# Optimization experiments

Measured on AMD Instinct MI355X. Metric: run time of the kernel, lower is better.

The kernel has to match this reference:

```python
import jax, jax.numpy as jnp
import numpy as np

N, E, CIN, H, HEADS, B = 50000, 800000, 16, 64, 3, 64
D0 = HEADS * H            # conv1 out (heads concatenated) = 192
D1 = D0 + CIN             # x1 dim = 208
D2 = 2 * D1               # x2 dim = 416
MLP_IN = 3 * D2           # 1248
MLP_HID = MLP_IN // 2     # 624
EPS = 1e-5


def setup_inputs() -> dict:
    key = jax.random.key(0)
    ks = jax.random.split(key, 24)
    r = lambda k, s, sc=0.05: (jax.random.normal(k, s, dtype=jnp.float32) * sc)
    inp = {
        'x': jax.random.normal(ks[0], (N, CIN), dtype=jnp.float32),
        'edge_index': jax.random.randint(ks[1], (2, E), 0, N, dtype=jnp.int32),
        'edge_attr': jax.random.normal(ks[2], (E, 4), dtype=jnp.float32),
        'batch': jnp.sort(jax.random.randint(ks[3], (N,), 0, B, dtype=jnp.int32)),
        # conv1 (GeneralConv, heads=3, concat): msg/edge/self linears -> D0
        'W_msg1': r(ks[4], (CIN, D0)), 'b_msg1': jnp.zeros((D0,), jnp.float32),
        'W_edge1': r(ks[5], (4, D0)), 'b_edge1': jnp.zeros((D0,), jnp.float32),
        'W_self1': r(ks[6], (CIN, D0)), 'b_self1': jnp.zeros((D0,), jnp.float32),
        'g1': jnp.ones((D0,), jnp.float32), 'be1': jnp.zeros((D0,), jnp.float32),
        # conv2 (GeneralConv, heads=1, in==out -> identity self)
        'W_msg2': r(ks[7], (D1, D1)), 'b_msg2': jnp.zeros((D1,), jnp.float32),
        'W_edge2': r(ks[8], (4, D1)), 'b_edge2': jnp.zeros((D1,), jnp.float32),
        'g2': jnp.ones((D1,), jnp.float32), 'be2': jnp.zeros((D1,), jnp.float32),
        # MLP head
        'W_l1': r(ks[9], (MLP_IN, MLP_HID)), 'b_l1': jnp.zeros((MLP_HID,), jnp.float32),
        'alpha': jnp.asarray(0.25, jnp.float32),  # PReLU default
        'W_l2': r(ks[10], (MLP_HID, 2)), 'b_l2': jnp.zeros((2,), jnp.float32),
    }
    return inp


def _bn(h, g, b):
    m = h.mean(axis=0)
    v = h.var(axis=0)  # biased, like torch BatchNorm training mode
    return (h - m) * jax.lax.rsqrt(v + EPS) * g + b


def reference(x, edge_index, edge_attr, batch,
              W_msg1, b_msg1, W_edge1, b_edge1, W_self1, b_self1, g1, be1,
              W_msg2, b_msg2, W_edge2, b_edge2, g2, be2,
              W_l1, b_l1, alpha, W_l2, b_l2):
    src, dst = edge_index[0], edge_index[1]
    # conv1: gather -> linear msg + edge feature -> scatter-add -> + self linear
    m1 = x[src] @ W_msg1 + b_msg1 + edge_attr @ W_edge1 + b_edge1   # [E, D0]
    h1 = jax.ops.segment_sum(m1, dst, num_segments=N) + (x @ W_self1 + b_self1)
    h1 = _bn(h1, g1, be1)
    x1 = jnp.concatenate([h1, x], axis=1)                           # [N, D1]
    # conv2 (identity self-connection since in==out)
    m2 = x1[src] @ W_msg2 + b_msg2 + edge_attr @ W_edge2 + b_edge2  # [E, D1]
    h2 = jax.ops.segment_sum(m2, dst, num_segments=N) + x1
    h2 = _bn(h2, g2, be2)
    x2 = jnp.concatenate([h2, x1], axis=1)                          # [N, D2]
    # global add / mean / max pooling by graph id
    s = jax.ops.segment_sum(x2, batch, num_segments=B)
    cnt = jax.ops.segment_sum(jnp.ones((x2.shape[0], 1), x2.dtype), batch, num_segments=B)
    mean = s / jnp.maximum(cnt, 1.0)
    mx = jax.ops.segment_max(x2, batch, num_segments=B)
    pooled = jnp.concatenate([s, mx, mean], axis=1)                 # [B, 3*D2]
    # MLP head: Linear -> Dropout(0) -> PReLU -> Linear -> log_softmax
    h = pooled @ W_l1 + b_l1
    h = jnp.where(h >= 0, h, alpha * h)
    logits = h @ W_l2 + b_l2
    return jax.nn.log_softmax(logits, axis=-1)
```

## Files before the change

### kernel.cpp

```cpp
#include <hip/hip_runtime.h>

typedef __attribute__((ext_vector_type(8))) short short8;
typedef __attribute__((ext_vector_type(4))) float f32x4;
typedef unsigned short u16;
typedef unsigned int u32;

__device__ __forceinline__ u16 f2bf(float f) {
  u32 u = __float_as_uint(f);
  u = (u + 0x7fffu + ((u >> 16) & 1u)) >> 16;
  return (u16)u;
}
__device__ __forceinline__ float bf2f(u16 v) { return __uint_as_float((u32)v << 16); }
__device__ __forceinline__ void atomAddF(float* p, float v) { unsafeAtomicAdd(p, v); }
__device__ __forceinline__ void addp(float* v, u32 p) {
  v[0] += bf2f((u16)p);
  v[1] += bf2f((u16)(p >> 16));
}
__device__ __forceinline__ u32 encf(float f) {
  u32 u = __float_as_uint(f);
  return (u & 0x80000000u) ? ~u : (u | 0x80000000u);
}
__device__ __forceinline__ float decf(u32 u) {
  return (u & 0x80000000u) ? __uint_as_float(u ^ 0x80000000u) : __uint_as_float(~u);
}

__global__ void prep_k(const float* __restrict__ Wm1, const float* __restrict__ We1,
                       const float* __restrict__ Ws1, const float* __restrict__ Wm2,
                       const float* __restrict__ Wl1, const float* __restrict__ x,
                       const int* __restrict__ batch, u16* __restrict__ Wp1,
                       u16* __restrict__ Wp2, u16* __restrict__ Wp3,
                       u16* __restrict__ xbf, int* __restrict__ gstart,
                       int* __restrict__ gend, int* __restrict__ deg,
                       float* __restrict__ bns1p, float* __restrict__ bns2p,
                       float* __restrict__ psumg, u32* __restrict__ pmaxg,
                       u32* __restrict__ pming, int N, int E) {
  int tid = blockIdx.x * 256 + threadIdx.x;
  if (tid < 64 * 192) {
    int k = tid / 192, n = tid % 192;
    float v = 0.f;
    if (k < 16) v = Wm1[k * 192 + n];
    else if (k < 20) v = We1[(k - 16) * 192 + n];
    else if (k < 36) v = Ws1[(k - 20) * 192 + n];
    Wp1[((k >> 3) * 192 + n) * 8 + (k & 7)] = f2bf(v);
  }
  if (tid < 224 * 208) {
    int k = tid / 208, n = tid % 208;
    float v = (k < 208) ? Wm2[k * 208 + n] : 0.f;
    Wp2[((k >> 3) * 208 + n) * 8 + (k & 7)] = f2bf(v);
  }
  if (tid < N * 8) {
    float2 p = *(const float2*)(x + (size_t)tid * 2);
    *(u32*)(xbf + (size_t)tid * 2) = (u32)f2bf(p.x) | ((u32)f2bf(p.y) << 16);
  }
  if (tid < N) {
    int b = batch[tid];
    if (tid == 0 || batch[tid - 1] != b) gstart[b] = tid;
    if (tid == N - 1 || batch[tid + 1] != b) gend[b] = tid;
    deg[tid] = 0;
  }
  if (tid < 64 * 384) bns1p[tid] = 0.f;
  if (tid < 64 * 832) bns2p[tid] = 0.f;
  if (tid < 64 * 416) {
    psumg[tid] = 0.f;
    pmaxg[tid] = 0x007FFFFFu;
    pming[tid] = 0xFF800000u;
  }
  if (tid < 1248 * 624) {
    int k = tid / 624, n = tid % 624;
    Wp3[((size_t)(k >> 3) * 624 + n) * 8 + (k & 7)] = f2bf(Wl1[(size_t)k * 624 + n]);
  }
}

__global__ void count_k(const int* __restrict__ ei, int* __restrict__ deg,
                        int* __restrict__ ord, int E) {
  int e = blockIdx.x * 256 + threadIdx.x;
  if (e >= E) return;
  ord[e] = atomicAdd(&deg[ei[E + e]], 1);
}

__global__ void scanA_k(const int* __restrict__ deg, int* __restrict__ bsum, int N) {
  __shared__ int sh[256];
  int t = threadIdx.x;
  int i = blockIdx.x * 256 + t;
  sh[t] = (i < N) ? deg[i] : 0;
  __syncthreads();
  for (int off = 128; off > 0; off >>= 1) {
    if (t < off) sh[t] += sh[t + off];
    __syncthreads();
  }
  if (t == 0) bsum[blockIdx.x] = sh[0];
}

__global__ void scanC_k(const int* __restrict__ deg, const int* __restrict__ bsum,
                        int* __restrict__ rowptr, int N, int nb) {
  __shared__ int sb2[256];
  __shared__ int sh[256];
  int t = threadIdx.x;
  int bv = (t < nb) ? bsum[t] : 0;
  sb2[t] = bv;
  __syncthreads();
  for (int off = 1; off < 256; off <<= 1) {
    int u = (t >= off) ? sb2[t - off] : 0;
    __syncthreads();
    sb2[t] += u;
    __syncthreads();
  }
  int bpref = (blockIdx.x == 0) ? 0 : sb2[blockIdx.x - 1];
  int i = blockIdx.x * 256 + t;
  int d = (i < N) ? deg[i] : 0;
  sh[t] = d;
  __syncthreads();
  for (int off = 1; off < 256; off <<= 1) {
    int u = (t >= off) ? sh[t - off] : 0;
    __syncthreads();
    sh[t] += u;
    __syncthreads();
  }
  int excl = sh[t] - d + bpref;
  if (i < N) {
    rowptr[i] = excl;
    if (i == N - 1) rowptr[N] = excl + d;
  }
}

__global__ void scatter_k(const int* __restrict__ ei, const float* __restrict__ ea,
                          const int* __restrict__ ord, const int* __restrict__ rowptr,
                          int4* __restrict__ se16, int E) {
  int e = blockIdx.x * 256 + threadIdx.x;
  if (e >= E) return;
  int s = ei[e], d = ei[E + e];
  float4 w = *(const float4*)(ea + (size_t)e * 4);
  int slot = rowptr[d] + ord[e];
  int4 ent;
  ent.x = s;
  ent.y = (int)((u32)f2bf(w.x) | ((u32)f2bf(w.y) << 16));
  ent.z = (int)((u32)f2bf(w.z) | ((u32)f2bf(w.w) << 16));
  ent.w = 0;
  se16[slot] = ent;
}

__global__ void __launch_bounds__(256) conv1_k(
    const int4* __restrict__ se16, const int* __restrict__ rowptr,
    const u16* __restrict__ xbf, const u16* __restrict__ Bp,
    const float* __restrict__ bm1, const float* __restrict__ be1,
    const float* __restrict__ bs1, u16* __restrict__ acc1c, u16* __restrict__ h1bf,
    float* __restrict__ bns1p, const int* __restrict__ batch,
    float* __restrict__ psumg, u32* __restrict__ pmaxg, u32* __restrict__ pming, int N) {
  __shared__ __align__(16) u16 Uls[16][72];
  __shared__ float degls[16];
  int tid = threadIdx.x;
  int nl = tid >> 4, q = tid & 15;
  int n = blockIdx.x * 16 + nl;
  bool nval = n < N;
  int j0 = nval ? rowptr[n] : 0;
  int j1 = nval ? rowptr[n + 1] : 0;
  int base = blockIdx.x * 16;
  int gid_lo = batch[base];
  int gid_hi = batch[min(base + 15, N - 1)];
  bool uni = (gid_lo == gid_hi);
  float v[20];
#pragma unroll
  for (int i = 0; i < 20; ++i) v[i] = 0.f;
  {
    int j = j0 + q;
    bool a0 = j < j1, a1 = (j + 16) < j1;
    int jj0 = a0 ? j : 0;
    int jj1 = a1 ? (j + 16) : 0;
    int4 p0 = se16[jj0];
    int4 p1 = se16[jj1];
    const uint4* xs0 = (const uint4*)(xbf + (size_t)(a0 ? p0.x : 0) * 16);
    uint4 x00 = xs0[0], x01 = xs0[1];
    const uint4* xs1 = (const uint4*)(xbf + (size_t)(a1 ? p1.x : 0) * 16);
    uint4 x10 = xs1[0], x11 = xs1[1];
    if (a0) {
      addp(v + 0, x00.x); addp(v + 2, x00.y); addp(v + 4, x00.z); addp(v + 6, x00.w);
      addp(v + 8, x01.x); addp(v + 10, x01.y); addp(v + 12, x01.z); addp(v + 14, x01.w);
      addp(v + 16, (u32)p0.y); addp(v + 18, (u32)p0.z);
    }
    if (a1) {
      addp(v + 0, x10.x); addp(v + 2, x10.y); addp(v + 4, x10.z); addp(v + 6, x10.w);
      addp(v + 8, x11.x); addp(v + 10, x11.y); addp(v + 12, x11.z); addp(v + 14, x11.w);
      addp(v + 16, (u32)p1.y); addp(v + 18, (u32)p1.z);
    }
    for (j += 32; j < j1; j += 16) {
      int4 p = se16[j];
      const uint4* xs = (const uint4*)(xbf + (size_t)p.x * 16);
      uint4 x0 = xs[0], x1 = xs[1];
      addp(v + 0, x0.x); addp(v + 2, x0.y); addp(v + 4, x0.z); addp(v + 6, x0.w);
      addp(v + 8, x1.x); addp(v + 10, x1.y); addp(v + 12, x1.z); addp(v + 14, x1.w);
      addp(v + 16, (u32)p.y); addp(v + 18, (u32)p.z);
    }
  }
#pragma unroll
  for (int i = 0; i < 20; ++i) {
    v[i] += __shfl_xor(v[i], 1);
    v[i] += __shfl_xor(v[i], 2);
    v[i] += __shfl_xor(v[i], 4);
    v[i] += __shfl_xor(v[i], 8);
  }
  float degf = (float)(j1 - j0);
  const u16* xr = xbf + (size_t)n * 16;
  {
    u32 w2[2];
#pragma unroll
    for (int jj = 0; jj < 2; ++jj) {
      int t0 = q * 4 + 2 * jj, t1 = t0 + 1;
      u16 b0 = (t0 < 20) ? f2bf(v[t0]) : ((t0 < 36 && nval) ? xr[t0 - 20] : (u16)0);
      u16 b1 = (t1 < 20) ? f2bf(v[t1]) : ((t1 < 36 && nval) ? xr[t1 - 20] : (u16)0);
      w2[jj] = (u32)b0 | ((u32)b1 << 16);
    }
    *(uint2*)&Uls[nl][q * 4] = make_uint2(w2[0], w2[1]);
  }
  if (nval) {
    int t0 = q * 2, t1 = t0 + 1;
    float f0 = (t0 < 20) ? v[t0] : ((t0 == 20) ? degf : 0.f);
    float f1 = (t1 < 20) ? v[t1] : ((t1 == 20) ? degf : 0.f);
    *(u32*)(acc1c + (size_t)n * 32 + q * 2) = (u32)f2bf(f0) | ((u32)f2bf(f1) << 16);
  }
  if (q == 0) degls[nl] = degf;
  __syncthreads();
  int w = tid >> 6, lane = tid & 63, rc = lane & 15, qd = lane >> 4;
  int slice = (blockIdx.x & 63) * 384;
  for (int nt = w; nt < 12; nt += 4) {
    f32x4 acc = {0.f, 0.f, 0.f, 0.f};
#pragma unroll
    for (int kb = 0; kb < 2; ++kb) {
      short8 av = *(const short8*)&Uls[rc][kb * 32 + qd * 8];
      short8 bv = *(const short8*)(Bp + (size_t)((kb * 4 + qd) * 192 + nt * 16 + rc) * 8);
      acc = __builtin_amdgcn_mfma_f32_16x16x32_bf16(av, bv, acc, 0, 0, 0);
    }
    int col = nt * 16 + rc;
    float bb = bm1[col] + be1[col], bsv = bs1[col];
    float ps = 0.f, pq = 0.f;
    float sl = 0.f, mxl = -3.4e38f, mnl = 3.4e38f;
    float vv[4];
#pragma unroll
    for (int r = 0; r < 4; ++r) {
      int ml = qd * 4 + r;
      int m = blockIdx.x * 16 + ml;
      float val = acc[r] + degls[ml] * bb + bsv;
      u16 vb = f2bf(val);
      float vr = bf2f(vb);
      vv[r] = vr;
      if (m < N) {
        h1bf[(size_t)m * 192 + col] = vb;
        ps += val;
        pq += val * val;
        sl += vr;
        mxl = fmaxf(mxl, vr);
        mnl = fminf(mnl, vr);
      }
    }
    ps += __shfl_xor(ps, 16); ps += __shfl_xor(ps, 32);
    pq += __shfl_xor(pq, 16); pq += __shfl_xor(pq, 32);
    if (uni) {
      sl += __shfl_xor(sl, 16); sl += __shfl_xor(sl, 32);
      mxl = fmaxf(mxl, __shfl_xor(mxl, 16)); mxl = fmaxf(mxl, __shfl_xor(mxl, 32));
      mnl = fminf(mnl, __shfl_xor(mnl, 16)); mnl = fminf(mnl, __shfl_xor(mnl, 32));
    }
    if (qd == 0) {
      atomAddF(&bns1p[slice + col], ps);
      atomAddF(&bns1p[slice + 192 + col], pq);
      if (uni) {
        int pidx = gid_lo * 416 + 208 + col;
        atomAddF(&psumg[pidx], sl);
        atomicMax(&pmaxg[pidx], encf(mxl));
        atomicMin(&pming[pidx], encf(mnl));
      }
    }
    if (!uni) {
      int cg = -1;
      float rs = 0.f, rmx = -3.4e38f, rmn = 3.4e38f;
#pragma unroll
      for (int r = 0; r < 4; ++r) {
        int m = blockIdx.x * 16 + qd * 4 + r;
        if (m >= N) continue;
        int g = batch[m];
        if (g != cg) {
          if (cg >= 0) {
            int pidx = cg * 416 + 208 + col;
            atomAddF(&psumg[pidx], rs);
            atomicMax(&pmaxg[pidx], encf(rmx));
            atomicMin(&pming[pidx], encf(rmn));
          }
          cg = g; rs = 0.f; rmx = -3.4e38f; rmn = 3.4e38f;
        }
        rs += vv[r];
        rmx = fmaxf(rmx, vv[r]);
        rmn = fminf(rmn, vv[r]);
      }
      if (cg >= 0) {
        int pidx = cg * 416 + 208 + col;
        atomAddF(&psumg[pidx], rs);
        atomicMax(&pmaxg[pidx], encf(rmx));
        atomicMin(&pming[pidx], encf(rmn));
      }
    }
  }
  if (tid < 16) {
    int c = tid;
    int rows = min(16, N - base);
    if (uni) {
      float s = 0.f, mx = -3.4e38f, mn = 3.4e38f;
      for (int ml = 0; ml < rows; ++ml) {
        float vx = bf2f(Uls[ml][20 + c]);
        s += vx;
        mx = fmaxf(mx, vx);
        mn = fminf(mn, vx);
      }
      int pidx = gid_lo * 416 + 400 + c;
      atomAddF(&psumg[pidx], s);
      atomicMax(&pmaxg[pidx], encf(mx));
      atomicMin(&pming[pidx], encf(mn));
    } else {
      int cg = -1;
      float rs = 0.f, rmx = -3.4e38f, rmn = 3.4e38f;
      for (int ml = 0; ml < rows; ++ml) {
        int g = batch[base + ml];
        if (g != cg) {
          if (cg >= 0) {
            int pidx = cg * 416 + 400 + c;
            atomAddF(&psumg[pidx], rs);
            atomicMax(&pmaxg[pidx], encf(rmx));
            atomicMin(&pming[pidx], encf(rmn));
          }
          cg = g; rs = 0.f; rmx = -3.4e38f; rmn = 3.4e38f;
        }
        float vx = bf2f(Uls[ml][20 + c]);
        rs += vx;
        rmx = fmaxf(rmx, vx);
        rmn = fminf(rmn, vx);
      }
      if (cg >= 0) {
        int pidx = cg * 416 + 400 + c;
        atomAddF(&psumg[pidx], rs);
        atomicMax(&pmaxg[pidx], encf(rmx));
        atomicMin(&pming[pidx], encf(rmn));
      }
    }
  }
}

__global__ void bnfin1_k(const float* __restrict__ bns1p, const float* __restrict__ g1,
                         const float* __restrict__ bta1, float Ninv,
                         float* __restrict__ aff1) {
  int c = threadIdx.x;
  if (c >= 192) return;
  float sm = 0.f, sq = 0.f;
  for (int k = 0; k < 64; ++k) {
    sm += bns1p[k * 384 + c];
    sq += bns1p[k * 384 + 192 + c];
  }
  float m1 = sm * Ninv;
  float var = sq * Ninv - m1 * m1;
  float s1 = g1[c] * rsqrtf(var + 1e-5f);
  aff1[c] = s1;
  aff1[192 + c] = bta1[c] - m1 * s1;
}

__global__ void __launch_bounds__(256) conv2_k(
    const int4* __restrict__ se16, const int* __restrict__ rowptr,
    const u16* __restrict__ acc1c, const u16* __restrict__ h1bf,
    const u16* __restrict__ xbf, const u16* __restrict__ Bp1, const u16* __restrict__ Bp2,
    const float* __restrict__ bm1, const float* __restrict__ be1,
    const float* __restrict__ bs1, const float* __restrict__ aff1,
    const float* __restrict__ We2, const float* __restrict__ bm2,
    const float* __restrict__ be2, float* __restrict__ bns2p,
    const int* __restrict__ batch, float* __restrict__ psumg,
    u32* __restrict__ pmaxg, u32* __restrict__ pming, int N) {
  __shared__ __align__(16) u16 Uls[16][72];
  __shared__ __align__(16) u16 Vls[16][232];
  __shared__ __align__(16) u16 X1ls[16][208];
  __shared__ float degls[16], sdegls[16], eals[16][4];
  int tid = threadIdx.x;
  int nl = tid >> 4, q = tid & 15;
  int n = blockIdx.x * 16 + nl;
  bool nval = n < N;
  int j0 = nval ? rowptr[n] : 0;
  int j1 = nval ? rowptr[n + 1] : 0;
  int base = blockIdx.x * 16;
  int gid_lo = batch[base];
  int gid_hi = batch[min(base + 15, N - 1)];
  bool uni = (gid_lo == gid_hi);

  uint4 sg0, sg1, sgx;
  int r0 = tid / 24, c0 = tid % 24;
  int r1 = (tid + 256) / 24, c1 = (tid + 256) % 24;
  {
    int gr = base + r0;
    sg0 = (gr < N) ? *(const uint4*)(h1bf + (size_t)gr * 192 + c0 * 8)
                   : make_uint4(0, 0, 0, 0);
  }
  if (tid < 128) {
    int gr = base + r1;
    sg1 = (gr < N) ? *(const uint4*)(h1bf + (size_t)gr * 192 + c1 * 8)
                   : make_uint4(0, 0, 0, 0);
  }
  if (tid < 32) {
    int gr = base + (tid >> 1);
    sgx = (gr < N) ? *(const uint4*)(xbf + (size_t)gr * 16 + (tid & 1) * 8)
                   : make_uint4(0, 0, 0, 0);
  }

  float v[21];
#pragma unroll
  for (int i = 0; i < 21; ++i) v[i] = 0.f;
  {
    int j = j0 + q;
    bool a0 = j < j1, a1 = (j + 16) < j1;
    int jj0 = a0 ? j : 0;
    int jj1 = a1 ? (j + 16) : 0;
    int4 p0 = se16[jj0];
    int4 p1 = se16[jj1];
    const uint4* cr0 = (const uint4*)(acc1c + (size_t)(a0 ? p0.x : 0) * 32);
    uint4 c00 = cr0[0], c01 = cr0[1], c02 = cr0[2];
    const uint4* cr1 = (const uint4*)(acc1c + (size_t)(a1 ? p1.x : 0) * 32);
    uint4 c10 = cr1[0], c11 = cr1[1], c12 = cr1[2];
    if (a0) {
      addp(v + 0, c00.x); addp(v + 2, c00.y); addp(v + 4, c00.z); addp(v + 6, c00.w);
      addp(v + 8, c01.x); addp(v + 10, c01.y); addp(v + 12, c01.z); addp(v + 14, c01.w);
      addp(v + 16, c02.x); addp(v + 18, c02.y);
      v[20] += bf2f((u16)c02.z);
    }
    if (a1) {
      addp(v + 0, c10.x); addp(v + 2, c10.y); addp(v + 4, c10.z); addp(v + 6, c10.w);
      addp(v + 8, c11.x); addp(v + 10, c11.y); addp(v + 12, c11.z); addp(v + 14, c11.w);
      addp(v + 16, c12.x); addp(v + 18, c12.y);
      v[20] += bf2f((u16)c12.z);
    }
    for (j += 32; j < j1; j += 16) {
      int s = se16[j].x;
      const uint4* cr = (const uint4*)(acc1c + (size_t)s * 32);
      uint4 c0 = cr[0], c1 = cr[1], c2 = cr[2];
      addp(v + 0, c0.x); addp(v + 2, c0.y); addp(v + 4, c0.z); addp(v + 6, c0.w);
      addp(v + 8, c1.x); addp(v + 10, c1.y); addp(v + 12, c1.z); addp(v + 14, c1.w);
      addp(v + 16, c2.x); addp(v + 18, c2.y);
      v[20] += bf2f((u16)c2.z);
    }
  }

  *(uint4*)&X1ls[r0][c0 * 8] = sg0;
  if (tid < 128) *(uint4*)&X1ls[r1][c1 * 8] = sg1;
  if (tid < 32) *(uint4*)&X1ls[tid >> 1][192 + (tid & 1) * 8] = sgx;

#pragma unroll
  for (int i = 0; i < 21; ++i) {
    v[i] += __shfl_xor(v[i], 1);
    v[i] += __shfl_xor(v[i], 2);
    v[i] += __shfl_xor(v[i], 4);
    v[i] += __shfl_xor(v[i], 8);
  }
  const u16* selfr = acc1c + (size_t)n * 32;
  {
    u32 w2[2];
#pragma unroll
    for (int jj = 0; jj < 2; ++jj) {
      int t0 = q * 4 + 2 * jj, t1 = t0 + 1;
      u16 b0 = (t0 < 20) ? f2bf(v[t0]) : ((t0 < 36 && nval) ? selfr[t0 - 20] : (u16)0);
      u16 b1 = (t1 < 20) ? f2bf(v[t1]) : ((t1 < 36 && nval) ? selfr[t1 - 20] : (u16)0);
      w2[jj] = (u32)b0 | ((u32)b1 << 16);
    }
    *(uint2*)&Uls[nl][q * 4] = make_uint2(w2[0], w2[1]);
  }
  {
    int t0 = q * 2, t1 = t0 + 1;
    u16 b0 = (t0 < 16 && nval) ? selfr[t0] : (u16)0;
    u16 b1 = (t1 < 16 && nval) ? selfr[t1] : (u16)0;
    *(u32*)&Vls[nl][192 + q * 2] = (u32)b0 | ((u32)b1 << 16);
  }
  if (q == 0) sdegls[nl] = v[20];
  if (q == 1) degls[nl] = nval ? bf2f(selfr[20]) : 0.f;
  if (q == 2) {
#pragma unroll
    for (int k = 0; k < 4; ++k) eals[nl][k] = nval ? bf2f(selfr[16 + k]) : 0.f;
  }
  __syncthreads();
  int w = tid >> 6, lane = tid & 63, rc = lane & 15, qd = lane >> 4;
  for (int nt = w; nt < 12; nt += 4) {
    f32x4 acc = {0.f, 0.f, 0.f, 0.f};
#pragma unroll
    for (int kb = 0; kb < 2; ++kb) {
      short8 av = *(const short8*)&Uls[rc][kb * 32 + qd * 8];
      short8 bv = *(const short8*)(Bp1 + (size_t)((kb * 4 + qd) * 192 + nt * 16 + rc) * 8);
      acc = __builtin_amdgcn_mfma_f32_16x16x32_bf16(av, bv, acc, 0, 0, 0);
    }
    int col = nt * 16 + rc;
    float s1 = aff1[col], t1 = aff1[192 + col];
    float bb = bm1[col] + be1[col], bsv = bs1[col];
#pragma unroll
    for (int r = 0; r < 4; ++r) {
      int ml = qd * 4 + r;
      float qv = acc[r] + sdegls[ml] * bb + degls[ml] * bsv;
      Vls[ml][col] = f2bf(qv * s1 + degls[ml] * t1);
    }
  }
  __syncthreads();
  int slice = (blockIdx.x & 63) * 832;
  for (int nt = w; nt < 13; nt += 4) {
    f32x4 acc = {0.f, 0.f, 0.f, 0.f};
#pragma unroll
    for (int kb = 0; kb < 7; ++kb) {
      short8 av = *(const short8*)&Vls[rc][kb * 32 + qd * 8];
      short8 bv = *(const short8*)(Bp2 + (size_t)((kb * 4 + qd) * 208 + nt * 16 + rc) * 8);
      acc = __builtin_amdgcn_mfma_f32_16x16x32_bf16(av, bv, acc, 0, 0, 0);
    }
    int col = nt * 16 + rc;
    float w0 = We2[col], w1 = We2[208 + col], w2 = We2[416 + col], w3 = We2[624 + col];
    float bb2 = bm2[col] + be2[col];
    bool c192 = col < 192;
    float s1 = c192 ? aff1[col] : 0.f;
    float t1 = c192 ? aff1[192 + col] : 0.f;
    float ps = 0.f, pq = 0.f;
    float sl = 0.f, mxl = -3.4e38f, mnl = 3.4e38f;
    float vv[4];
#pragma unroll
    for (int r = 0; r < 4; ++r) {
      int ml = qd * 4 + r;
      int m = blockIdx.x * 16 + ml;
      bool mv = m < N;
      float x1 = bf2f(X1ls[ml][col]);
      if (c192) x1 = x1 * s1 + t1;
      float val = acc[r] + eals[ml][0] * w0 + eals[ml][1] * w1 + eals[ml][2] * w2 +
                  eals[ml][3] * w3 + degls[ml] * bb2 + x1;
      vv[r] = val;
      if (mv) {
        ps += val;
        pq += val * val;
        sl += val;
        mxl = fmaxf(mxl, val);
        mnl = fminf(mnl, val);
      }
    }
    ps += __shfl_xor(ps, 16); ps += __shfl_xor(ps, 32);
    pq += __shfl_xor(pq, 16); pq += __shfl_xor(pq, 32);
    if (uni) {
      sl += __shfl_xor(sl, 16); sl += __shfl_xor(sl, 32);
      mxl = fmaxf(mxl, __shfl_xor(mxl, 16)); mxl = fmaxf(mxl, __shfl_xor(mxl, 32));
      mnl = fminf(mnl, __shfl_xor(mnl, 16)); mnl = fminf(mnl, __shfl_xor(mnl, 32));
    }
    if (qd == 0) {
      atomAddF(&bns2p[slice + col], ps);
      atomAddF(&bns2p[slice + 416 + col], pq);
      if (uni) {
        int pidx = gid_lo * 416 + col;
        atomAddF(&psumg[pidx], sl);
        atomicMax(&pmaxg[pidx], encf(mxl));
        atomicMin(&pming[pidx], encf(mnl));
      }
    }
    if (!uni) {
      int cg = -1;
      float rs = 0.f, rmx = -3.4e38f, rmn = 3.4e38f;
#pragma unroll
      for (int r = 0; r < 4; ++r) {
        int m = blockIdx.x * 16 + qd * 4 + r;
        if (m >= N) continue;
        int g = batch[m];
        if (g != cg) {
          if (cg >= 0) {
            int pidx = cg * 416 + col;
            atomAddF(&psumg[pidx], rs);
            atomicMax(&pmaxg[pidx], encf(rmx));
            atomicMin(&pming[pidx], encf(rmn));
          }
          cg = g; rs = 0.f; rmx = -3.4e38f; rmn = 3.4e38f;
        }
        rs += vv[r];
        rmx = fmaxf(rmx, vv[r]);
        rmn = fminf(rmn, vv[r]);
      }
      if (cg >= 0) {
        int pidx = cg * 416 + col;
        atomAddF(&psumg[pidx], rs);
        atomicMax(&pmaxg[pidx], encf(rmx));
        atomicMin(&pming[pidx], encf(rmn));
      }
    }
  }
}

__global__ void pooledprep_k(const float* __restrict__ psumg, const u32* __restrict__ pmaxg,
                             const u32* __restrict__ pming,
                             const int* __restrict__ gstart, const int* __restrict__ gend,
                             const float* __restrict__ bns2p, const float* __restrict__ aff1,
                             const float* __restrict__ g2, const float* __restrict__ bta2,
                             float Ninv, u16* __restrict__ Apool) {
  __shared__ float scs[416], shs[416];
  int b = blockIdx.x, t = threadIdx.x;
  for (int f = t; f < 416; f += 256) {
    float sc, sh;
    if (f < 208) {
      float sm = 0.f, sq = 0.f;
      for (int k = 0; k < 64; ++k) {
        sm += bns2p[k * 832 + f];
        sq += bns2p[k * 832 + 416 + f];
      }
      float m2 = sm * Ninv;
      float var = sq * Ninv - m2 * m2;
      sc = g2[f] * rsqrtf(var + 1e-5f);
      sh = bta2[f] - m2 * sc;
    } else if (f < 400) {
      sc = aff1[f - 208];
      sh = aff1[192 + (f - 208)];
    } else {
      sc = 1.f;
      sh = 0.f;
    }
    scs[f] = sc;
    shs[f] = sh;
  }
  __syncthreads();
  int cnt = gend[b] - gstart[b] + 1;
  float inv = 1.f / (float)max(cnt, 1);
  for (int f = t; f < 416; f += 256) {
    float s = psumg[b * 416 + f];
    float mx = decf(pmaxg[b * 416 + f]);
    float mn = decf(pming[b * 416 + f]);
    float sc = scs[f], sh = shs[f];
    float sumf = sc * s + (float)cnt * sh;
    float mxf = (sc >= 0.f) ? sc * mx + sh : sc * mn + sh;
    u16* row = Apool + (size_t)b * 1248;
    row[f] = f2bf(sumf);
    row[416 + f] = f2bf((cnt > 0) ? mxf : 0.f);
    row[832 + f] = f2bf(sumf * inv);
  }
}

__global__ void __launch_bounds__(256) mlpgemm_k(const u16* __restrict__ A,
                                                 const u16* __restrict__ Bp,
                                                 const float* __restrict__ b1,
                                                 const float* __restrict__ al,
                                                 float* __restrict__ hid) {
  __shared__ __align__(16) float part[3][64][4];
  int tid = threadIdx.x;
  int w = tid >> 6, lane = tid & 63;
  int mt = blockIdx.x, nt = blockIdx.y;
  int rc = lane & 15, qd = lane >> 4;
  f32x4 acc = {0.f, 0.f, 0.f, 0.f};
  const u16* Ap = A + (size_t)(mt * 16 + rc) * 1248 + qd * 8;
  const u16* Bq = Bp + (size_t)(qd * 624 + nt * 16 + rc) * 8;
  for (int kb = w; kb < 39; kb += 4) {
    short8 av = *(const short8*)(Ap + kb * 32);
    short8 bv = *(const short8*)(Bq + (size_t)kb * 4 * 624 * 8);
    acc = __builtin_amdgcn_mfma_f32_16x16x32_bf16(av, bv, acc, 0, 0, 0);
  }
  if (w > 0) *(f32x4*)&part[w - 1][lane][0] = acc;
  __syncthreads();
  if (w == 0) {
#pragma unroll
    for (int j = 0; j < 3; ++j) {
      f32x4 p = *(const f32x4*)&part[j][lane][0];
      acc[0] += p[0]; acc[1] += p[1]; acc[2] += p[2]; acc[3] += p[3];
    }
    int col = nt * 16 + rc;
    float bb = b1[col], alpha = al[0];
    int m0 = mt * 16 + qd * 4;
#pragma unroll
    for (int r = 0; r < 4; ++r) {
      float v = acc[r] + bb;
      hid[(size_t)(m0 + r) * 624 + col] = (v >= 0.f) ? v : alpha * v;
    }
  }
}

__global__ void head_k(const float* __restrict__ hid, const float* __restrict__ W2,
                       const float* __restrict__ b2, float* __restrict__ out) {
  int b = blockIdx.x, t = threadIdx.x;
  float p0 = 0.f, p1 = 0.f;
  for (int k = t; k < 624; k += 64) {
    float h = hid[(size_t)b * 624 + k];
    p0 += h * W2[k * 2];
    p1 += h * W2[k * 2 + 1];
  }
#pragma unroll
  for (int off = 32; off > 0; off >>= 1) {
    p0 += __shfl_down(p0, off);
    p1 += __shfl_down(p1, off);
  }
  if (t == 0) {
    float l0 = p0 + b2[0], l1 = p1 + b2[1];
    float m = fmaxf(l0, l1);
    float lse = m + logf(expf(l0 - m) + expf(l1 - m));
    out[b * 2] = l0 - lse;
    out[b * 2 + 1] = l1 - lse;
  }
}

extern "C" void kernel_launch(void* const* d_in, const int* in_sizes, int n_in,
                              void* d_out, int out_size, void* d_ws, size_t ws_size,
                              hipStream_t stream) {
  const float* x = (const float*)d_in[0];
  const int* ei = (const int*)d_in[1];
  const float* ea = (const float*)d_in[2];
  const int* batch = (const int*)d_in[3];
  const float* Wm1 = (const float*)d_in[4];
  const float* bm1 = (const float*)d_in[5];
  const float* We1 = (const float*)d_in[6];
  const float* be1 = (const float*)d_in[7];
  const float* Ws1 = (const float*)d_in[8];
  const float* bs1 = (const float*)d_in[9];
  const float* g1 = (const float*)d_in[10];
  const float* bta1 = (const float*)d_in[11];
  const float* Wm2 = (const float*)d_in[12];
  const float* bm2 = (const float*)d_in[13];
  const float* We2 = (const float*)d_in[14];
  const float* be2 = (const float*)d_in[15];
  const float* g2 = (const float*)d_in[16];
  const float* bta2 = (const float*)d_in[17];
  const float* Wl1 = (const float*)d_in[18];
  const float* bl1 = (const float*)d_in[19];
  const float* alpha = (const float*)d_in[20];
  const float* Wl2 = (const float*)d_in[21];
  const float* bl2 = (const float*)d_in[22];
  float* out = (float*)d_out;

  const int N = in_sizes[3];
  const int E = in_sizes[2] / 4;
  const int nb = (N + 255) / 256;
  const float Ninv = 1.f / (float)N;

  float* ws = (float*)d_ws;
  size_t o = 0;
  u16* acc1c = (u16*)(ws + o); o += (size_t)N * 16;
  u16* h1bf = (u16*)(ws + o);  o += (size_t)N * 96;
  u16* xbf = (u16*)(ws + o);   o += (size_t)N * 8;
  u16* Wp1 = (u16*)(ws + o);   o += 6144;
  u16* Wp2 = (u16*)(ws + o);   o += 23296;
  u16* Wp3 = (u16*)(ws + o);   o += 389376;
  u16* Apool = (u16*)(ws + o); o += 39936;
  float* hid = ws + o;    o += 64 * 624;
  float* bns1p = ws + o;  o += 64 * 384;
  float* bns2p = ws + o;  o += 64 * 832;
  float* aff1 = ws + o;   o += 384;
  float* psumg = ws + o;  o += 64 * 416;
  u32* pmaxg = (u32*)(ws + o); o += 64 * 416;
  u32* pming = (u32*)(ws + o); o += 64 * 416;
  int* gstart = (int*)(ws + o); o += 64;
  int* gend = (int*)(ws + o);   o += 64;
  int* deg = (int*)(ws + o);    o += N;
  int* rowptr = (int*)(ws + o); o += N + 1;
  int* ord = (int*)(ws + o);    o += E;
  int* bsum = (int*)(ws + o);   o += 256;
  o = (o + 3) & ~(size_t)3;
  int4* se16 = (int4*)(ws + o); o += (size_t)4 * E;

  const int gconv = (N + 15) / 16;
  prep_k<<<(E + 255) / 256, 256, 0, stream>>>(Wm1, We1, Ws1, Wm2, Wl1, x, batch, Wp1, Wp2,
                                              Wp3, xbf, gstart, gend, deg, bns1p, bns2p,
                                              psumg, pmaxg, pming, N, E);
  count_k<<<(E + 255) / 256, 256, 0, stream>>>(ei, deg, ord, E);
  scanA_k<<<nb, 256, 0, stream>>>(deg, bsum, N);
  scanC_k<<<nb, 256, 0, stream>>>(deg, bsum, rowptr, N, nb);
  scatter_k<<<(E + 255) / 256, 256, 0, stream>>>(ei, ea, ord, rowptr, se16, E);
  conv1_k<<<gconv, 256, 0, stream>>>(se16, rowptr, xbf, Wp1, bm1, be1, bs1, acc1c, h1bf,
                                     bns1p, batch, psumg, pmaxg, pming, N);
  bnfin1_k<<<1, 256, 0, stream>>>(bns1p, g1, bta1, Ninv, aff1);
  conv2_k<<<gconv, 256, 0, stream>>>(se16, rowptr, acc1c, h1bf, xbf, Wp1, Wp2, bm1, be1,
                                     bs1, aff1, We2, bm2, be2, bns2p, batch, psumg,
                                     pmaxg, pming, N);
  pooledprep_k<<<64, 256, 0, stream>>>(psumg, pmaxg, pming, gstart, gend, bns2p, aff1,
                                       g2, bta2, Ninv, Apool);
  mlpgemm_k<<<dim3(4, 39), 256, 0, stream>>>(Apool, Wp3, bl1, alpha, hid);
  head_k<<<64, 64, 0, stream>>>(hid, Wl2, bl2, out);
}
```

Baseline: 279.5 us.

## Fuse degree count into prep, single-pass scan, and pooled prep into MLP GEMM

Folds the edge degree counting into the prep kernel, with deg zeroed by a memset, and replaces the two-kernel block scan with one kernel in which each block recomputes its prefix by summing all earlier degrees. It also fuses the pooled-feature preparation into the MLP GEMM, building the bf16 A tile in shared memory per block. The aim is to cut kernel launches and the Apool global round trip. In exchange, each block in the scan and GEMM does redundant work (the prefix sum over earlier degrees, and the BN2 statistic reduction repeated in all 156 GEMM blocks).

```diff
diff --git a/kernel.cpp b/kernel.cpp
--- a/kernel.cpp
+++ b/kernel.cpp
@@ -27,10 +27,11 @@
 __global__ void prep_k(const float* __restrict__ Wm1, const float* __restrict__ We1,
                        const float* __restrict__ Ws1, const float* __restrict__ Wm2,
                        const float* __restrict__ Wl1, const float* __restrict__ x,
-                       const int* __restrict__ batch, u16* __restrict__ Wp1,
-                       u16* __restrict__ Wp2, u16* __restrict__ Wp3,
-                       u16* __restrict__ xbf, int* __restrict__ gstart,
-                       int* __restrict__ gend, int* __restrict__ deg,
+                       const int* __restrict__ batch, const int* __restrict__ ei,
+                       u16* __restrict__ Wp1, u16* __restrict__ Wp2,
+                       u16* __restrict__ Wp3, u16* __restrict__ xbf,
+                       int* __restrict__ gstart, int* __restrict__ gend,
+                       int* __restrict__ deg, int* __restrict__ ord,
                        float* __restrict__ bns1p, float* __restrict__ bns2p,
                        float* __restrict__ psumg, u32* __restrict__ pmaxg,
                        u32* __restrict__ pming, int N, int E) {
@@ -56,7 +57,6 @@
     int b = batch[tid];
     if (tid == 0 || batch[tid - 1] != b) gstart[b] = tid;
     if (tid == N - 1 || batch[tid + 1] != b) gend[b] = tid;
-    deg[tid] = 0;
   }
   if (tid < 64 * 384) bns1p[tid] = 0.f;
   if (tid < 64 * 832) bns2p[tid] = 0.f;
@@ -69,44 +69,26 @@
     int k = tid / 624, n = tid % 624;
     Wp3[((size_t)(k >> 3) * 624 + n) * 8 + (k & 7)] = f2bf(Wl1[(size_t)k * 624 + n]);
   }
-}
-
-__global__ void count_k(const int* __restrict__ ei, int* __restrict__ deg,
-                        int* __restrict__ ord, int E) {
-  int e = blockIdx.x * 256 + threadIdx.x;
-  if (e >= E) return;
-  ord[e] = atomicAdd(&deg[ei[E + e]], 1);
-}
-
-__global__ void scanA_k(const int* __restrict__ deg, int* __restrict__ bsum, int N) {
+  if (tid < E) {
+    ord[tid] = atomicAdd(&deg[ei[E + tid]], 1);
+  }
+}
+
+__global__ void scan_k(const int* __restrict__ deg, int* __restrict__ rowptr, int N) {
+  __shared__ int red[256];
   __shared__ int sh[256];
   int t = threadIdx.x;
-  int i = blockIdx.x * 256 + t;
-  sh[t] = (i < N) ? deg[i] : 0;
+  int start = blockIdx.x * 256;
+  int acc = 0;
+  for (int idx = t; idx < start; idx += 256) acc += deg[idx];
+  red[t] = acc;
   __syncthreads();
   for (int off = 128; off > 0; off >>= 1) {
-    if (t < off) sh[t] += sh[t + off];
+    if (t < off) red[t] += red[t + off];
     __syncthreads();
   }
-  if (t == 0) bsum[blockIdx.x] = sh[0];
-}
-
-__global__ void scanC_k(const int* __restrict__ deg, const int* __restrict__ bsum,
-                        int* __restrict__ rowptr, int N, int nb) {
-  __shared__ int sb2[256];
-  __shared__ int sh[256];
-  int t = threadIdx.x;
-  int bv = (t < nb) ? bsum[t] : 0;
-  sb2[t] = bv;
-  __syncthreads();
-  for (int off = 1; off < 256; off <<= 1) {
-    int u = (t >= off) ? sb2[t - off] : 0;
-    __syncthreads();
-    sb2[t] += u;
-    __syncthreads();
-  }
-  int bpref = (blockIdx.x == 0) ? 0 : sb2[blockIdx.x - 1];
-  int i = blockIdx.x * 256 + t;
+  int bpref = red[0];
+  int i = start + t;
   int d = (i < N) ? deg[i] : 0;
   sh[t] = d;
   __syncthreads();
@@ -579,15 +561,20 @@
   }
 }
 
-__global__ void pooledprep_k(const float* __restrict__ psumg, const u32* __restrict__ pmaxg,
-                             const u32* __restrict__ pming,
-                             const int* __restrict__ gstart, const int* __restrict__ gend,
-                             const float* __restrict__ bns2p, const float* __restrict__ aff1,
-                             const float* __restrict__ g2, const float* __restrict__ bta2,
-                             float Ninv, u16* __restrict__ Apool) {
+__global__ void __launch_bounds__(256) mlpgemm_k(
+    const float* __restrict__ psumg, const u32* __restrict__ pmaxg,
+    const u32* __restrict__ pming, const int* __restrict__ gstart,
+    const int* __restrict__ gend, const float* __restrict__ bns2p,
+    const float* __restrict__ aff1, const float* __restrict__ g2,
+    const float* __restrict__ bta2, float Ninv, const u16* __restrict__ Bp,
+    const float* __restrict__ b1, const float* __restrict__ al,
+    float* __restrict__ hid) {
   __shared__ float scs[416], shs[416];
-  int b = blockIdx.x, t = threadIdx.x;
-  for (int f = t; f < 416; f += 256) {
+  __shared__ __align__(16) u16 Als[16][1256];
+  __shared__ __align__(16) float part[3][64][4];
+  int tid = threadIdx.x;
+  int mt = blockIdx.x, nt = blockIdx.y;
+  for (int f = tid; f < 416; f += 256) {
     float sc, sh;
     if (f < 208) {
       float sm = 0.f, sq = 0.f;
@@ -610,37 +597,28 @@
     shs[f] = sh;
   }
   __syncthreads();
-  int cnt = gend[b] - gstart[b] + 1;
-  float inv = 1.f / (float)max(cnt, 1);
-  for (int f = t; f < 416; f += 256) {
+  for (int e = tid; e < 16 * 416; e += 256) {
+    int g = e / 416, f = e % 416;
+    int b = mt * 16 + g;
+    int cnt = gend[b] - gstart[b] + 1;
+    float inv = 1.f / (float)max(cnt, 1);
     float s = psumg[b * 416 + f];
     float mx = decf(pmaxg[b * 416 + f]);
     float mn = decf(pming[b * 416 + f]);
     float sc = scs[f], sh = shs[f];
     float sumf = sc * s + (float)cnt * sh;
     float mxf = (sc >= 0.f) ? sc * mx + sh : sc * mn + sh;
-    u16* row = Apool + (size_t)b * 1248;
-    row[f] = f2bf(sumf);
-    row[416 + f] = f2bf((cnt > 0) ? mxf : 0.f);
-    row[832 + f] = f2bf(sumf * inv);
-  }
-}
-
-__global__ void __launch_bounds__(256) mlpgemm_k(const u16* __restrict__ A,
-                                                 const u16* __restrict__ Bp,
-                                                 const float* __restrict__ b1,
-                                                 const float* __restrict__ al,
-                                                 float* __restrict__ hid) {
-  __shared__ __align__(16) float part[3][64][4];
-  int tid = threadIdx.x;
+    Als[g][f] = f2bf(sumf);
+    Als[g][416 + f] = f2bf((cnt > 0) ? mxf : 0.f);
+    Als[g][832 + f] = f2bf(sumf * inv);
+  }
+  __syncthreads();
   int w = tid >> 6, lane = tid & 63;
-  int mt = blockIdx.x, nt = blockIdx.y;
   int rc = lane & 15, qd = lane >> 4;
   f32x4 acc = {0.f, 0.f, 0.f, 0.f};
-  const u16* Ap = A + (size_t)(mt * 16 + rc) * 1248 + qd * 8;
   const u16* Bq = Bp + (size_t)(qd * 624 + nt * 16 + rc) * 8;
   for (int kb = w; kb < 39; kb += 4) {
-    short8 av = *(const short8*)(Ap + kb * 32);
+    short8 av = *(const short8*)&Als[rc][kb * 32 + qd * 8];
     short8 bv = *(const short8*)(Bq + (size_t)kb * 4 * 624 * 8);
     acc = __builtin_amdgcn_mfma_f32_16x16x32_bf16(av, bv, acc, 0, 0, 0);
   }
@@ -727,7 +705,6 @@
   u16* Wp1 = (u16*)(ws + o);   o += 6144;
   u16* Wp2 = (u16*)(ws + o);   o += 23296;
   u16* Wp3 = (u16*)(ws + o);   o += 389376;
-  u16* Apool = (u16*)(ws + o); o += 39936;
   float* hid = ws + o;    o += 64 * 624;
   float* bns1p = ws + o;  o += 64 * 384;
   float* bns2p = ws + o;  o += 64 * 832;
@@ -740,17 +717,16 @@
   int* deg = (int*)(ws + o);    o += N;
   int* rowptr = (int*)(ws + o); o += N + 1;
   int* ord = (int*)(ws + o);    o += E;
-  int* bsum = (int*)(ws + o);   o += 256;
   o = (o + 3) & ~(size_t)3;
   int4* se16 = (int4*)(ws + o); o += (size_t)4 * E;
 
   const int gconv = (N + 15) / 16;
-  prep_k<<<(E + 255) / 256, 256, 0, stream>>>(Wm1, We1, Ws1, Wm2, Wl1, x, batch, Wp1, Wp2,
-                                              Wp3, xbf, gstart, gend, deg, bns1p, bns2p,
-                                              psumg, pmaxg, pming, N, E);
-  count_k<<<(E + 255) / 256, 256, 0, stream>>>(ei, deg, ord, E);
-  scanA_k<<<nb, 256, 0, stream>>>(deg, bsum, N);
-  scanC_k<<<nb, 256, 0, stream>>>(deg, bsum, rowptr, N, nb);
+  hipMemsetAsync(deg, 0, (size_t)N * sizeof(int), stream);
+  prep_k<<<(E + 255) / 256, 256, 0, stream>>>(Wm1, We1, Ws1, Wm2, Wl1, x, batch, ei,
+                                              Wp1, Wp2, Wp3, xbf, gstart, gend, deg,
+                                              ord, bns1p, bns2p, psumg, pmaxg, pming,
+                                              N, E);
+  scan_k<<<nb, 256, 0, stream>>>(deg, rowptr, N);
   scatter_k<<<(E + 255) / 256, 256, 0, stream>>>(ei, ea, ord, rowptr, se16, E);
   conv1_k<<<gconv, 256, 0, stream>>>(se16, rowptr, xbf, Wp1, bm1, be1, bs1, acc1c, h1bf,
                                      bns1p, batch, psumg, pmaxg, pming, N);
@@ -758,8 +734,7 @@
   conv2_k<<<gconv, 256, 0, stream>>>(se16, rowptr, acc1c, h1bf, xbf, Wp1, Wp2, bm1, be1,
                                      bs1, aff1, We2, bm2, be2, bns2p, batch, psumg,
                                      pmaxg, pming, N);
-  pooledprep_k<<<64, 256, 0, stream>>>(psumg, pmaxg, pming, gstart, gend, bns2p, aff1,
-                                       g2, bta2, Ninv, Apool);
-  mlpgemm_k<<<dim3(4, 39), 256, 0, stream>>>(Apool, Wp3, bl1, alpha, hid);
+  mlpgemm_k<<<dim3(4, 39), 256, 0, stream>>>(psumg, pmaxg, pming, gstart, gend, bns2p,
+                                             aff1, g2, bta2, Ninv, Wp3, bl1, alpha, hid);
   head_k<<<64, 64, 0, stream>>>(hid, Wl2, bl2, out);
 }
```

Result: slower. 318.6 us (+14.0%).
